# Optimization experiments

Measured on AMD Instinct MI355X. Metric: run time of the kernel, lower is better.

The kernel has to match this reference:

```python
import jax, jax.numpy as jnp
import numpy as np

DIM = 256
HEADS = 8
HD = DIM // HEADS        # head_dim = 32
WS = 8                   # window_size (Wh = Ww = 8)
NEXP = 8                 # num_experts
HID = 128                # attr_hidden_size (router hidden)
SCALE = HD ** -0.5


def _window_partition(x, ws):
    # (B, H, W, C) -> (B * H//ws * W//ws, ws, ws, C)
    B, H, W, C = x.shape
    x = x.reshape(B, H // ws, ws, W // ws, ws, C)
    return x.transpose(0, 1, 3, 2, 4, 5).reshape(-1, ws, ws, C)


def _window_reverse(w, ws, B, H, W):
    # inverse of _window_partition
    C = w.shape[-1]
    x = w.reshape(B, H // ws, W // ws, ws, ws, C)
    return x.transpose(0, 1, 3, 2, 4, 5).reshape(B, H, W, C)


def _rope2(x):
    # 2D rotary embedding over a window: x (B*, Wh, Ww, d).
    # First d/2 channels rotated by row position, last d/2 by column position.
    B, Wh, Ww, d = x.shape
    d2 = d // 2

    def angles(L, dd):
        inv = 1.0 / (10000.0 ** (jnp.arange(0, dd, 2, dtype=jnp.float32) / dd))
        return jnp.arange(L, dtype=jnp.float32)[:, None] * inv[None, :]  # (L, dd//2)

    def rotate(v, ang, bshape):
        # v: (B, Wh, Ww, dd) pairs interleaved; ang broadcast as bshape
        p = v.reshape(*v.shape[:-1], -1, 2)
        c = jnp.cos(ang).reshape(bshape)
        s = jnp.sin(ang).reshape(bshape)
        o0 = p[..., 0] * c - p[..., 1] * s
        o1 = p[..., 0] * s + p[..., 1] * c
        return jnp.stack([o0, o1], axis=-1).reshape(v.shape)

    ah = angles(Wh, d2)  # (Wh, d2//2)
    aw = angles(Ww, d2)  # (Ww, d2//2)
    xh = rotate(x[..., :d2], ah, (1, Wh, 1, d2 // 2))
    xw = rotate(x[..., d2:], aw, (1, 1, Ww, d2 // 2))
    return jnp.concatenate([xh, xw], axis=-1)


def _moe_linear(xf, routes, w, b):
    # Top-1 dispatch: per-expert dense GEMM, masked select (jit-safe, static shapes).
    # xf: (T, in), routes: (T,) int, w: (E, out, in), b: (E, out)
    out = jnp.zeros((xf.shape[0], w.shape[1]), xf.dtype)
    for i in range(w.shape[0]):
        y = xf @ w[i].T + b[i]
        out = jnp.where((routes == i)[:, None], y, out)
    return out


def setup_inputs() -> dict:
    key = jax.random.key(0)
    ks = jax.random.split(key, 8)
    sc = 0.02
    return {
        "x": jax.random.normal(ks[0], (8, 64, 64, DIM), jnp.float32),
        "router_w1": jax.random.normal(ks[1], (HID, DIM), jnp.float32) * sc,
        "router_b1": jnp.zeros((HID,), jnp.float32),
        "router_w2": jax.random.normal(ks[2], (NEXP, HID), jnp.float32) * sc,
        "router_b2": jnp.zeros((NEXP,), jnp.float32),
        "qkv_w": jax.random.normal(ks[3], (NEXP, 3 * DIM, DIM), jnp.float32) * sc,
        "qkv_b": jnp.zeros((NEXP, 3 * DIM), jnp.float32),
        "proj_w": jax.random.normal(ks[4], (NEXP, DIM, DIM), jnp.float32) * sc,
        "proj_b": jnp.zeros((NEXP, DIM), jnp.float32),
    }


def reference(x, router_w1, router_b1, router_w2, router_b2,
              qkv_w, qkv_b, proj_w, proj_b):
    Bs, H, W, C = x.shape
    xf = x.reshape(-1, C)  # (T, C), T = Bs*H*W

    # --- Top-1 router (eval mode: no noise, no token dropping) ---
    h = jax.nn.relu(xf @ router_w1.T + router_b1)
    router_logits = h @ router_w2.T + router_b2          # (T, E)
    router_probs = jax.nn.softmax(router_logits, axis=-1)
    route_prob_max = jnp.max(router_probs, axis=-1)       # (T,)
    routes = jnp.argmax(router_probs, axis=-1)            # (T,)

    # --- per-expert QKV projection (grouped dispatch) ---
    qkv = _moe_linear(xf, routes, qkv_w, qkv_b)           # (T, 3C)
    qkv = qkv.reshape(Bs, H, W, 3 * C)

    # --- window partition (shift=0, dilated=1 -> no roll, mask=None) ---
    qw = _window_partition(qkv, WS).reshape(-1, WS * WS, 3 * C)
    B_, N, _ = qw.shape
    qkv5 = qw.reshape(B_, N, 3, HEADS, HD).transpose(2, 0, 3, 1, 4)  # (3,B_,h,N,hd)
    q, k, v = qkv5[0], qkv5[1], qkv5[2]

    # --- RoPE on q, k over the 2D window ---
    q = _rope2(q.reshape(-1, WS, WS, HD)).reshape(B_, HEADS, N, HD)
    k = _rope2(k.reshape(-1, WS, WS, HD)).reshape(B_, HEADS, N, HD)

    # --- windowed attention (moe_mask is all zeros in eval: no drops) ---
    attn = jax.nn.softmax((q * SCALE) @ k.swapaxes(-2, -1), axis=-1)  # (B_,h,N,N)
    out = (attn @ v).swapaxes(1, 2).reshape(B_, N, C)

    # --- window reverse ---
    out = _window_reverse(out.reshape(-1, WS, WS, C), WS, Bs, H, W)

    # --- per-expert output projection + Switch-style prob scaling ---
    of = _moe_linear(out.reshape(-1, C), routes, proj_w, proj_b)
    of = of * route_prob_max[:, None]
    return of.reshape(Bs, H, W, C)
```

## Files before the change

### kernel.cpp

```cpp
#include <hip/hip_runtime.h>
#include <hip/hip_bf16.h>

typedef unsigned short u16;
typedef unsigned int u32;
typedef __attribute__((ext_vector_type(8))) short short8;
typedef __attribute__((ext_vector_type(4))) float f32x4;

#define T_TOK 32768
#define SCALE_ATT 0.17677669529663687f

__device__ __forceinline__ u16 f2bf(float f){
  u32 u = __float_as_uint(f);
  u32 r = u + 0x7fffu + ((u >> 16) & 1u);
  return (u16)(r >> 16);
}
__device__ __forceinline__ float bf2f(u16 h){
  return __uint_as_float(((u32)h) << 16);
}

__device__ __forceinline__ int xcd_swz(int flat, int nwg){
  return (flat & 7) * (nwg >> 3) + (flat >> 3);
}

__device__ __forceinline__ void gl16(const u16* g, u16* l){
  __builtin_amdgcn_global_load_lds(
      (const __attribute__((address_space(1))) u32*)g,
      (__attribute__((address_space(3))) u32*)l, 16, 0, 0);
}

__global__ __launch_bounds__(256) void k_prep_w1(
    const float* __restrict__ rw1, u16* __restrict__ w1h, u16* __restrict__ w1l)
{
  int i = blockIdx.x * 256 + threadIdx.x;
  float4 v = ((const float4*)rw1)[i];
  ushort4 h, l;
  h.x = f2bf(v.x); h.y = f2bf(v.y); h.z = f2bf(v.z); h.w = f2bf(v.w);
  l.x = f2bf(v.x - bf2f(h.x)); l.y = f2bf(v.y - bf2f(h.y));
  l.z = f2bf(v.z - bf2f(h.z)); l.w = f2bf(v.w - bf2f(h.w));
  ((ushort4*)w1h)[i] = h;
  ((ushort4*)w1l)[i] = l;
}

__global__ __launch_bounds__(256) void k_router(
    const float* __restrict__ x, const u16* __restrict__ w1h, const u16* __restrict__ w1l,
    const float* __restrict__ b1, const float* __restrict__ w2, const float* __restrict__ b2,
    int* __restrict__ routes, float* __restrict__ pmax, int* __restrict__ hist,
    u16* __restrict__ x_bf,
    const float* __restrict__ qkvw, u16* __restrict__ qw_bf,
    const float* __restrict__ projw, u16* __restrict__ pw_bf)
{
  __shared__ __align__(16) char smem[64*132*4];
  int tid = threadIdx.x;

  if (blockIdx.x >= 512){
    int b = blockIdx.x - 512;
    if (b < 1536){
      int i = b * 256 + tid;
      float4 v = ((const float4*)qkvw)[i];
      ushort4 o;
      o.x = f2bf(v.x); o.y = f2bf(v.y); o.z = f2bf(v.z); o.w = f2bf(v.w);
      ((ushort4*)qw_bf)[i] = o;
    } else {
      int i = (b - 1536) * 256 + tid;
      float4 v = ((const float4*)projw)[i];
      ushort4 o;
      o.x = f2bf(v.x); o.y = f2bf(v.y); o.z = f2bf(v.z); o.w = f2bf(v.w);
      ((ushort4*)pw_bf)[i] = o;
    }
    return;
  }

  u16* Ah = (u16*)smem;
  u16* Al = Ah + 2560;
  u16* Bh = Al + 2560;
  u16* Bl = Bh + 5120;
  float* Hs = (float*)smem;
  __shared__ int lhist[8];

  int t0 = blockIdx.x * 64;
  int wv = tid >> 6, lane = tid & 63, quad = lane >> 4, l16 = lane & 15;
  if (tid < 8) lhist[tid] = 0;

  int arow = tid >> 2, acg = tid & 3;
  int brow = tid >> 1, bhalf = tid & 1;

  f32x4 acc[4][2];
  #pragma unroll
  for (int i = 0; i < 4; ++i)
    #pragma unroll
    for (int j = 0; j < 2; ++j)
      #pragma unroll
      for (int rr = 0; rr < 4; ++rr) acc[i][j][rr] = 0.f;

  const float* gx_base = x + (size_t)(t0 + arow) * 256 + acg * 8;
  u16* gxb_base = x_bf + (size_t)(t0 + arow) * 256 + acg * 8;
  const u16* gwh_base = w1h + (size_t)brow * 256 + bhalf * 16;
  const u16* gwl_base = w1l + (size_t)brow * 256 + bhalf * 16;

  float4 v0 = *(const float4*)gx_base;
  float4 v1 = *(const float4*)(gx_base + 4);
  uint4 wh0 = *(const uint4*)(gwh_base);
  uint4 wh1 = *(const uint4*)(gwh_base + 8);
  uint4 wl0 = *(const uint4*)(gwl_base);
  uint4 wl1 = *(const uint4*)(gwl_base + 8);

  for (int kt = 0; kt < 8; ++kt){
    ushort4 h0, h1, l0, l1;
    h0.x = f2bf(v0.x); h0.y = f2bf(v0.y); h0.z = f2bf(v0.z); h0.w = f2bf(v0.w);
    h1.x = f2bf(v1.x); h1.y = f2bf(v1.y); h1.z = f2bf(v1.z); h1.w = f2bf(v1.w);
    l0.x = f2bf(v0.x - bf2f(h0.x)); l0.y = f2bf(v0.y - bf2f(h0.y));
    l0.z = f2bf(v0.z - bf2f(h0.z)); l0.w = f2bf(v0.w - bf2f(h0.w));
    l1.x = f2bf(v1.x - bf2f(h1.x)); l1.y = f2bf(v1.y - bf2f(h1.y));
    l1.z = f2bf(v1.z - bf2f(h1.z)); l1.w = f2bf(v1.w - bf2f(h1.w));
    *(ushort4*)(gxb_base + kt*32)     = h0;
    *(ushort4*)(gxb_base + kt*32 + 4) = h1;
    __syncthreads();
    *(ushort4*)&Ah[arow*40 + acg*8    ] = h0;
    *(ushort4*)&Ah[arow*40 + acg*8 + 4] = h1;
    *(ushort4*)&Al[arow*40 + acg*8    ] = l0;
    *(ushort4*)&Al[arow*40 + acg*8 + 4] = l1;
    *(uint4*)&Bh[brow*40 + bhalf*16    ] = wh0;
    *(uint4*)&Bh[brow*40 + bhalf*16 + 8] = wh1;
    *(uint4*)&Bl[brow*40 + bhalf*16    ] = wl0;
    *(uint4*)&Bl[brow*40 + bhalf*16 + 8] = wl1;
    __syncthreads();
    if (kt < 7){
      v0  = *(const float4*)(gx_base + (kt+1)*32);
      v1  = *(const float4*)(gx_base + (kt+1)*32 + 4);
      wh0 = *(const uint4*)(gwh_base + (kt+1)*32);
      wh1 = *(const uint4*)(gwh_base + (kt+1)*32 + 8);
      wl0 = *(const uint4*)(gwl_base + (kt+1)*32);
      wl1 = *(const uint4*)(gwl_base + (kt+1)*32 + 8);
    }
    short8 ah[4], al[4], bhf[2], blf[2];
    #pragma unroll
    for (int i = 0; i < 4; ++i){
      ah[i] = *(const short8*)&Ah[(i*16 + l16)*40 + quad*8];
      al[i] = *(const short8*)&Al[(i*16 + l16)*40 + quad*8];
    }
    #pragma unroll
    for (int j = 0; j < 2; ++j){
      bhf[j] = *(const short8*)&Bh[(wv*32 + j*16 + l16)*40 + quad*8];
      blf[j] = *(const short8*)&Bl[(wv*32 + j*16 + l16)*40 + quad*8];
    }
    #pragma unroll
    for (int i = 0; i < 4; ++i)
      #pragma unroll
      for (int j = 0; j < 2; ++j){
        acc[i][j] = __builtin_amdgcn_mfma_f32_16x16x32_bf16(ah[i], bhf[j], acc[i][j], 0, 0, 0);
        acc[i][j] = __builtin_amdgcn_mfma_f32_16x16x32_bf16(ah[i], blf[j], acc[i][j], 0, 0, 0);
        acc[i][j] = __builtin_amdgcn_mfma_f32_16x16x32_bf16(al[i], bhf[j], acc[i][j], 0, 0, 0);
      }
  }
  __syncthreads();

  #pragma unroll
  for (int i = 0; i < 4; ++i)
    #pragma unroll
    for (int j = 0; j < 2; ++j){
      int col = wv*32 + j*16 + l16;
      float bb = b1[col];
      #pragma unroll
      for (int rr = 0; rr < 4; ++rr){
        float h = acc[i][j][rr] + bb;
        Hs[(i*16 + quad*4 + rr)*132 + col] = h > 0.f ? h : 0.f;
      }
    }
  __syncthreads();

  #pragma unroll
  for (int pass = 0; pass < 2; ++pass){
    int mtok = (tid >> 3) + pass * 32;
    int e = tid & 7;
    const float4* w2r = (const float4*)(w2 + e * 128);
    float l = b2[e];
    #pragma unroll
    for (int k4 = 0; k4 < 32; ++k4){
      float4 w = w2r[k4];
      int k = k4 * 4;
      l = fmaf(Hs[mtok*132+k  ], w.x, l);
      l = fmaf(Hs[mtok*132+k+1], w.y, l);
      l = fmaf(Hs[mtok*132+k+2], w.z, l);
      l = fmaf(Hs[mtok*132+k+3], w.w, l);
    }
    float mv = l; int mi = e;
    #pragma unroll
    for (int off = 1; off < 8; off <<= 1){
      float ov = __shfl_xor(mv, off, 64);
      int   oi = __shfl_xor(mi, off, 64);
      if (ov > mv || (ov == mv && oi < mi)){ mv = ov; mi = oi; }
    }
    float sum = expf(l - mv);
    #pragma unroll
    for (int off = 1; off < 8; off <<= 1) sum += __shfl_xor(sum, off, 64);
    if (e == 0){
      int t = t0 + mtok;
      routes[t] = mi;
      pmax[t] = 1.0f / sum;
      atomicAdd(&lhist[mi], 1);
    }
  }
  __syncthreads();
  if (tid < 8) hist[blockIdx.x * 8 + tid] = lhist[tid];
}

__global__ __launch_bounds__(256) void k_scatter(
    const int* __restrict__ routes, const int* __restrict__ hist,
    int* __restrict__ sorted, int* __restrict__ rank, int* __restrict__ offs)
{
  __shared__ int s_tot[8], s_pre[8], so[9], lc[8];
  int tid = threadIdx.x, b = blockIdx.x;
  if (tid < 8){ s_tot[tid] = 0; s_pre[tid] = 0; lc[tid] = 0; }
  __syncthreads();
  int e8 = tid & 7, r0 = tid >> 3;
  int tot = 0, pre = 0;
  for (int rb = r0; rb < 512; rb += 32){
    int v = hist[rb * 8 + e8];
    tot += v;
    if (rb < b * 4) pre += v;
  }
  atomicAdd(&s_tot[e8], tot);
  atomicAdd(&s_pre[e8], pre);
  __syncthreads();
  if (tid == 0){
    int o = 0; so[0] = 0;
    #pragma unroll
    for (int e = 0; e < 8; ++e){ o += ((s_tot[e] + 127) >> 7) << 7; so[e+1] = o; }
  }
  __syncthreads();
  int t = b * 256 + tid;
  int e = routes[t];
  int rl = atomicAdd(&lc[e], 1);
  int pos = so[e] + s_pre[e] + rl;
  sorted[pos] = t;
  rank[t] = pos;
  if (b == 0){
    if (tid < 9) offs[tid] = so[tid];
    #pragma unroll
    for (int e2 = 0; e2 < 8; ++e2)
      for (int i = so[e2] + s_tot[e2] + tid; i < so[e2+1]; i += 256) sorted[i] = -1;
  }
}

template<int NOUT, bool PROJ, int NB, int NWG>
__global__ __launch_bounds__(256) void k_gemm(
    const u16* __restrict__ A, const u16* __restrict__ W,
    const float* __restrict__ bias, const int* __restrict__ sidx,
    const int* __restrict__ offs, const float* __restrict__ pmax,
    u16* __restrict__ outb, float* __restrict__ outf)
{
  __shared__ __align__(1024) u16 As[3][4096];
  __shared__ __align__(1024) u16 Bs[3][4096];
  int tid = threadIdx.x;
  int flat = blockIdx.y * NB + blockIdx.x;
  int logical = xcd_swz(flat, NWG);
  int m0 = (logical / NB) * 128;
  int n0 = (logical % NB) * 128;
  int total = offs[8];
  if (m0 >= total) return;
  int e = 0;
  #pragma unroll
  for (int i = 1; i < 8; ++i) if (m0 >= offs[i]) e = i;

  int wv = tid >> 6, lane = tid & 63, quad = lane >> 4, l16 = lane & 15;
  int wrow = (wv >> 1) * 64, wcol = (wv & 1) * 64;

  int srow = wv*16 + (lane >> 2);
  int cg = (lane & 3) ^ ((srow >> 1) & 3);
  const u16 *ag0, *ag1;
  if (PROJ){
    ag0 = A + (size_t)(m0 + srow) * 256 + cg * 8;
    ag1 = A + (size_t)(m0 + srow + 64) * 256 + cg * 8;
  } else {
    int tA0 = sidx[m0 + srow];      if (tA0 < 0) tA0 = 0;
    int tA1 = sidx[m0 + srow + 64]; if (tA1 < 0) tA1 = 0;
    ag0 = A + (size_t)tA0 * 256 + cg * 8;
    ag1 = A + (size_t)tA1 * 256 + cg * 8;
  }
  int pc = (srow >> 4) + (srow & 15) * 4;
  const u16* bg0 = W + ((size_t)e * NOUT + n0 + pc) * 256 + cg * 8;
  const u16* bg1 = W + ((size_t)e * NOUT + n0 + 64 + pc) * 256 + cg * 8;

  f32x4 acc[4][4];
  #pragma unroll
  for (int i = 0; i < 4; ++i)
    #pragma unroll
    for (int j = 0; j < 4; ++j)
      #pragma unroll
      for (int r = 0; r < 4; ++r) acc[i][j][r] = 0.f;

  int qsw8 = (quad ^ ((l16 >> 1) & 3)) * 8;

#define STAGE_KT(kt, buf) do { \
    u16* a_lo = (u16*)((char*)&As[(buf)][0] + wv*1024); \
    u16* b_lo = (u16*)((char*)&Bs[(buf)][0] + wv*1024); \
    gl16(ag0 + (kt)*32, a_lo); \
    gl16(ag1 + (kt)*32, (u16*)((char*)a_lo + 4096)); \
    gl16(bg0 + (kt)*32, b_lo); \
    gl16(bg1 + (kt)*32, (u16*)((char*)b_lo + 4096)); \
  } while(0)

  STAGE_KT(0, 0);
  STAGE_KT(1, 1);

  #pragma unroll
  for (int kt = 0; kt < 8; ++kt){
    const int cur = kt % 3;
    if (kt < 7) asm volatile("s_waitcnt vmcnt(4) lgkmcnt(0)" ::: "memory");
    else        asm volatile("s_waitcnt vmcnt(0) lgkmcnt(0)" ::: "memory");
    __builtin_amdgcn_sched_barrier(0);
    __builtin_amdgcn_s_barrier();
    __builtin_amdgcn_sched_barrier(0);
    if (kt < 6) STAGE_KT(kt+2, (kt+2)%3);
    short8 af[4], bfv[4];
    #pragma unroll
    for (int i = 0; i < 4; ++i)
      af[i] = *(const short8*)&As[cur][(wrow + i*16 + l16)*32 + qsw8];
    #pragma unroll
    for (int j = 0; j < 4; ++j)
      bfv[j] = *(const short8*)&Bs[cur][(wcol + j*16 + l16)*32 + qsw8];
    #pragma unroll
    for (int i = 0; i < 4; ++i)
      #pragma unroll
      for (int j = 0; j < 4; ++j)
        acc[i][j] = __builtin_amdgcn_mfma_f32_16x16x32_bf16(af[i], bfv[j], acc[i][j], 0, 0, 0);
  }
#undef STAGE_KT

  float4 bj4 = *(const float4*)&bias[e*NOUT + n0 + wcol + l16*4];
  if (PROJ){
    #pragma unroll
    for (int i = 0; i < 4; ++i){
      #pragma unroll
      for (int ri = 0; ri < 4; ++ri){
        int row = wrow + i*16 + quad*4 + ri;
        int t = sidx[m0 + row];
        if (t < 0) continue;
        float pm = pmax[t];
        float4 ov;
        ov.x = (acc[i][0][ri] + bj4.x) * pm;
        ov.y = (acc[i][1][ri] + bj4.y) * pm;
        ov.z = (acc[i][2][ri] + bj4.z) * pm;
        ov.w = (acc[i][3][ri] + bj4.w) * pm;
        *(float4*)&outf[(size_t)t * NOUT + n0 + wcol + l16*4] = ov;
      }
    }
  } else {
    int col0 = n0 + wcol + l16*4;
    bool isqk = (col0 < 512);
    float inv0 = 0.f, inv1 = 0.f;
    float qsc = (col0 < 256) ? SCALE_ATT : 1.0f;
    if (isqk){
      int p0 = (col0 & 15) >> 1;
      inv0 = __expf(-1.1512925465f * (float)p0);
      inv1 = inv0 * 0.31622776601683794f;
    }
    int sel  = col0 >> 8;
    int head = (col0 >> 5) & 7;
    int ch   = col0 & 31;
    size_t hb = ((size_t)(sel * 8 + head) * 512) * 2048 + ch;
    #pragma unroll
    for (int i = 0; i < 4; ++i){
      #pragma unroll
      for (int ri = 0; ri < 4; ++ri){
        int row = wrow + i*16 + quad*4 + ri;
        int t = sidx[m0 + row];
        if (t < 0) continue;
        float vx = acc[i][0][ri] + bj4.x;
        float vy = acc[i][1][ri] + bj4.y;
        float vz = acc[i][2][ri] + bj4.z;
        float vw = acc[i][3][ri] + bj4.w;
        if (isqk){
          float pos = (float)((col0 & 16) ? (t & 7) : ((t >> 6) & 7));
          float a0r = pos * inv0, a1r = pos * inv1;
          float s0, c0s, s1, c1s;
          __sincosf(a0r, &s0, &c0s);
          __sincosf(a1r, &s1, &c1s);
          float r0 = (vx*c0s - vy*s0) * qsc;
          float r1 = (vx*s0 + vy*c0s) * qsc;
          float r2 = (vz*c1s - vw*s1) * qsc;
          float r3 = (vz*s1 + vw*c1s) * qsc;
          vx = r0; vy = r1; vz = r2; vw = r3;
        }
        int win = (t >> 12) * 64 + ((t >> 9) & 7) * 8 + ((t >> 3) & 7);
        int n   = ((t >> 6) & 7) * 8 + (t & 7);
        uint2 ov;
        ov.x = (u32)f2bf(vx) | ((u32)f2bf(vy) << 16);
        ov.y = (u32)f2bf(vz) | ((u32)f2bf(vw) << 16);
        *(uint2*)&outb[hb + (size_t)win * 2048 + n * 32] = ov;
      }
    }
  }
}

__global__ __launch_bounds__(64, 3) void k_attn(const u16* __restrict__ qkv,
                                                const int* __restrict__ rank,
                                                u16* __restrict__ attn_s)
{
  __shared__ __align__(16) u16 Ps[64*72];
  __shared__ __align__(16) u16 Vt[32*72];

  int lane = threadIdx.x;
  int quad = lane >> 4, l16 = lane & 15;
  int wh = xcd_swz(blockIdx.x, 4096);
  int head = wh >> 9, win = wh & 511;
  int b = win >> 6, wy = (win >> 3) & 7, wx = win & 7;
  int tb = b*4096 + wy*512 + wx*8;

  const u16* qbase = qkv + (size_t)(head * 512 + win) * 2048;
  const u16* kbase = qbase + (size_t)8 * 512 * 2048;
  const u16* vbase = qbase + (size_t)16 * 512 * 2048;

  int rk[4][4];
  #pragma unroll
  for (int i = 0; i < 4; ++i)
    #pragma unroll
    for (int rr = 0; rr < 4; ++rr){
      int m = i*16 + quad*4 + rr;
      rk[i][rr] = rank[tb + (m >> 3) * 64 + (m & 7)];
    }

  short8 qf[4], kf[4];
  #pragma unroll
  for (int i = 0; i < 4; ++i){
    qf[i] = *(const short8*)(qbase + (i*16 + l16)*32 + quad*8);
    kf[i] = *(const short8*)(kbase + (i*16 + l16)*32 + quad*8);
  }
  uint4 va[4];
  #pragma unroll
  for (int h = 0; h < 4; ++h)
    va[h] = *(const uint4*)(vbase + h*512 + l16*32 + quad*8);

  f32x4 sa[4][4];
  #pragma unroll
  for (int i = 0; i < 4; ++i)
    #pragma unroll
    for (int j = 0; j < 4; ++j){
      #pragma unroll
      for (int rr = 0; rr < 4; ++rr) sa[i][j][rr] = 0.f;
      sa[i][j] = __builtin_amdgcn_mfma_f32_16x16x32_bf16(qf[i], kf[j], sa[i][j], 0, 0, 0);
    }

  f32x4 rs[4];
  #pragma unroll
  for (int i = 0; i < 4; ++i)
    #pragma unroll
    for (int rr = 0; rr < 4; ++rr){
      float e0 = __expf(sa[i][0][rr]);
      float e1 = __expf(sa[i][1][rr]);
      float e2 = __expf(sa[i][2][rr]);
      float e3 = __expf(sa[i][3][rr]);
      rs[i][rr] = (e0 + e1) + (e2 + e3);
      uint2 pk;
      pk.x = (u32)f2bf(e0) | ((u32)f2bf(e1) << 16);
      pk.y = (u32)f2bf(e2) | ((u32)f2bf(e3) << 16);
      *(uint2*)&Ps[(i*16 + quad*4 + rr)*72 + l16*4] = pk;
    }
  #pragma unroll
  for (int i = 0; i < 4; ++i)
    #pragma unroll
    for (int rr = 0; rr < 4; ++rr){
      #pragma unroll
      for (int off = 1; off < 16; off <<= 1)
        rs[i][rr] += __shfl_xor(rs[i][rr], off, 64);
    }

  u32* vu = (u32*)va;
  #pragma unroll
  for (int h = 0; h < 4; ++h){
    int pn = l16 * 4 + h;
    #pragma unroll
    for (int w = 0; w < 4; ++w){
      u32 vv = vu[h*4 + w];
      Vt[(quad*8 + 2*w    )*72 + pn] = (u16)(vv & 0xffff);
      Vt[(quad*8 + 2*w + 1)*72 + pn] = (u16)(vv >> 16);
    }
  }

  f32x4 oa[4][2];
  #pragma unroll
  for (int i = 0; i < 4; ++i)
    #pragma unroll
    for (int rr = 0; rr < 4; ++rr){ oa[i][0][rr] = 0.f; oa[i][1][rr] = 0.f; }
  #pragma unroll
  for (int ks = 0; ks < 2; ++ks){
    short8 vf0 = *(const short8*)&Vt[(     l16)*72 + ks*32 + quad*8];
    short8 vf1 = *(const short8*)&Vt[(16 + l16)*72 + ks*32 + quad*8];
    #pragma unroll
    for (int i = 0; i < 4; ++i){
      short8 pf = *(const short8*)&Ps[(i*16 + l16)*72 + ks*32 + quad*8];
      oa[i][0] = __builtin_amdgcn_mfma_f32_16x16x32_bf16(pf, vf0, oa[i][0], 0, 0, 0);
      oa[i][1] = __builtin_amdgcn_mfma_f32_16x16x32_bf16(pf, vf1, oa[i][1], 0, 0, 0);
    }
  }

  #pragma unroll
  for (int i = 0; i < 4; ++i)
    #pragma unroll
    for (int rr = 0; rr < 4; ++rr){
      float inv = __builtin_amdgcn_rcpf(rs[i][rr]);
      int pos = rk[i][rr];
      u16* op = attn_s + (size_t)pos * 256 + head * 32 + l16;
      op[0]  = f2bf(oa[i][0][rr] * inv);
      op[16] = f2bf(oa[i][1][rr] * inv);
    }
}

extern "C" void kernel_launch(void* const* d_in, const int* in_sizes, int n_in,
                              void* d_out, int out_size, void* d_ws, size_t ws_size,
                              hipStream_t stream){
  const float* x     = (const float*)d_in[0];
  const float* rw1   = (const float*)d_in[1];
  const float* rb1   = (const float*)d_in[2];
  const float* rw2   = (const float*)d_in[3];
  const float* rb2   = (const float*)d_in[4];
  const float* qkvw  = (const float*)d_in[5];
  const float* qkvb  = (const float*)d_in[6];
  const float* projw = (const float*)d_in[7];
  const float* projb = (const float*)d_in[8];
  float* out = (float*)d_out;

  char* ws = (char*)d_ws;
  u16*   x_bf    = (u16*)(ws);
  u16*   qkv_bf  = (u16*)(ws + 16777216);
  u16*   w1h     = (u16*)(ws + 67108864);
  u16*   w1l     = w1h + 32768;
  u16*   attn_s  = (u16*)(ws + 67108864);
  u16*   qw_bf   = (u16*)(ws + 84410368);
  u16*   pw_bf   = (u16*)(ws + 87556096);
  int*   routes  = (int*)(ws + 88604672);
  float* pmaxp   = (float*)(ws + 88735744);
  int*   sorted  = (int*)(ws + 88866816);
  int*   rank    = (int*)(ws + 89001984);
  int*   hist    = (int*)(ws + 89133056);
  int*   offs    = (int*)(ws + 89149440);

  k_prep_w1<<<32, 256, 0, stream>>>(rw1, w1h, w1l);
  k_router<<<2560, 256, 0, stream>>>(x, w1h, w1l, rb1, rw2, rb2, routes, pmaxp, hist,
                                     x_bf, qkvw, qw_bf, projw, pw_bf);
  k_scatter<<<128, 256, 0, stream>>>(routes, hist, sorted, rank, offs);
  k_gemm<768, false, 6, 1584><<<dim3(6, 264), 256, 0, stream>>>(
      x_bf, qw_bf, qkvb, sorted, offs, nullptr, qkv_bf, nullptr);
  k_attn<<<4096, 64, 0, stream>>>(qkv_bf, rank, attn_s);
  k_gemm<256, true, 2, 528><<<dim3(2, 264), 256, 0, stream>>>(
      attn_s, pw_bf, projb, sorted, offs, pmaxp, nullptr, out);
}
```

Before: 195.3 us.

## Widen grouped GEMM tile to 128x256 with interleaved column mapping

Doubles the N tile of the expert-grouped GEMM from 128 to 256 columns, so each wave now accumulates a 64x128 block and the A tile is reused across twice as many output columns. B rows are loaded with a permuted column mapping so each lane owns 8 contiguous output columns, which allows 16-byte bf16 stores and handles four RoPE frequency pairs per lane. The grid is halved, and launch bounds now request one block per CU. Register and LDS use per block grow, which lowers occupancy and may hurt latency hiding, and the smaller grid leaves fewer blocks to spread across CUs.

```diff
diff --git a/kernel.cpp b/kernel.cpp
--- a/kernel.cpp
+++ b/kernel.cpp
@@ -243,19 +243,19 @@
 }
 
 template<int NOUT, bool PROJ, int NB, int NWG>
-__global__ __launch_bounds__(256) void k_gemm(
+__global__ __launch_bounds__(256, 1) void k_gemm(
     const u16* __restrict__ A, const u16* __restrict__ W,
     const float* __restrict__ bias, const int* __restrict__ sidx,
     const int* __restrict__ offs, const float* __restrict__ pmax,
     u16* __restrict__ outb, float* __restrict__ outf)
 {
   __shared__ __align__(1024) u16 As[3][4096];
-  __shared__ __align__(1024) u16 Bs[3][4096];
+  __shared__ __align__(1024) u16 Bs[3][8192];
   int tid = threadIdx.x;
   int flat = blockIdx.y * NB + blockIdx.x;
   int logical = xcd_swz(flat, NWG);
   int m0 = (logical / NB) * 128;
-  int n0 = (logical % NB) * 128;
+  int n0 = (logical % NB) * 256;
   int total = offs[8];
   if (m0 >= total) return;
   int e = 0;
@@ -263,7 +263,7 @@
   for (int i = 1; i < 8; ++i) if (m0 >= offs[i]) e = i;
 
   int wv = tid >> 6, lane = tid & 63, quad = lane >> 4, l16 = lane & 15;
-  int wrow = (wv >> 1) * 64, wcol = (wv & 1) * 64;
+  int wrow = (wv >> 1) * 64, wcol = (wv & 1) * 128;
 
   int srow = wv*16 + (lane >> 2);
   int cg = (lane & 3) ^ ((srow >> 1) & 3);
@@ -277,57 +277,67 @@
     ag0 = A + (size_t)tA0 * 256 + cg * 8;
     ag1 = A + (size_t)tA1 * 256 + cg * 8;
   }
-  int pc = (srow >> 4) + (srow & 15) * 4;
-  const u16* bg0 = W + ((size_t)e * NOUT + n0 + pc) * 256 + cg * 8;
-  const u16* bg1 = W + ((size_t)e * NOUT + n0 + 64 + pc) * 256 + cg * 8;
-
-  f32x4 acc[4][4];
-  #pragma unroll
-  for (int i = 0; i < 4; ++i)
-    #pragma unroll
-    for (int j = 0; j < 4; ++j)
+  int pcb = (srow & 15) * 8 + (srow >> 4);
+  const u16* bg0 = W + ((size_t)e * NOUT + n0 +       pcb    ) * 256 + cg * 8;
+  const u16* bg1 = W + ((size_t)e * NOUT + n0 +       pcb + 4) * 256 + cg * 8;
+  const u16* bg2 = W + ((size_t)e * NOUT + n0 + 128 + pcb    ) * 256 + cg * 8;
+  const u16* bg3 = W + ((size_t)e * NOUT + n0 + 128 + pcb + 4) * 256 + cg * 8;
+
+  f32x4 acc[4][8];
+  #pragma unroll
+  for (int i = 0; i < 4; ++i)
+    #pragma unroll
+    for (int j = 0; j < 8; ++j)
       #pragma unroll
       for (int r = 0; r < 4; ++r) acc[i][j][r] = 0.f;
 
   int qsw8 = (quad ^ ((l16 >> 1) & 3)) * 8;
 
 #define STAGE_KT(kt, buf) do { \
-    u16* a_lo = (u16*)((char*)&As[(buf)][0] + wv*1024); \
-    u16* b_lo = (u16*)((char*)&Bs[(buf)][0] + wv*1024); \
+    u16* a_lo = &As[(buf)][0] + wv*512; \
+    u16* b_lo = &Bs[(buf)][0] + wv*512; \
     gl16(ag0 + (kt)*32, a_lo); \
-    gl16(ag1 + (kt)*32, (u16*)((char*)a_lo + 4096)); \
+    gl16(ag1 + (kt)*32, a_lo + 2048); \
     gl16(bg0 + (kt)*32, b_lo); \
-    gl16(bg1 + (kt)*32, (u16*)((char*)b_lo + 4096)); \
+    gl16(bg1 + (kt)*32, b_lo + 2048); \
+    gl16(bg2 + (kt)*32, b_lo + 4096); \
+    gl16(bg3 + (kt)*32, b_lo + 6144); \
   } while(0)
 
   STAGE_KT(0, 0);
+  __builtin_amdgcn_sched_barrier(0);
   STAGE_KT(1, 1);
+  __builtin_amdgcn_sched_barrier(0);
 
   #pragma unroll
   for (int kt = 0; kt < 8; ++kt){
     const int cur = kt % 3;
-    if (kt < 7) asm volatile("s_waitcnt vmcnt(4) lgkmcnt(0)" ::: "memory");
+    if (kt < 7) asm volatile("s_waitcnt vmcnt(6) lgkmcnt(0)" ::: "memory");
     else        asm volatile("s_waitcnt vmcnt(0) lgkmcnt(0)" ::: "memory");
     __builtin_amdgcn_sched_barrier(0);
     __builtin_amdgcn_s_barrier();
     __builtin_amdgcn_sched_barrier(0);
-    if (kt < 6) STAGE_KT(kt+2, (kt+2)%3);
-    short8 af[4], bfv[4];
+    if (kt < 6){
+      STAGE_KT(kt+2, (kt+2)%3);
+      __builtin_amdgcn_sched_barrier(0);
+    }
+    short8 af[4];
     #pragma unroll
     for (int i = 0; i < 4; ++i)
       af[i] = *(const short8*)&As[cur][(wrow + i*16 + l16)*32 + qsw8];
     #pragma unroll
-    for (int j = 0; j < 4; ++j)
-      bfv[j] = *(const short8*)&Bs[cur][(wcol + j*16 + l16)*32 + qsw8];
-    #pragma unroll
-    for (int i = 0; i < 4; ++i)
-      #pragma unroll
-      for (int j = 0; j < 4; ++j)
-        acc[i][j] = __builtin_amdgcn_mfma_f32_16x16x32_bf16(af[i], bfv[j], acc[i][j], 0, 0, 0);
+    for (int j = 0; j < 8; ++j){
+      short8 bf = *(const short8*)&Bs[cur][(wcol + j*16 + l16)*32 + qsw8];
+      #pragma unroll
+      for (int i = 0; i < 4; ++i)
+        acc[i][j] = __builtin_amdgcn_mfma_f32_16x16x32_bf16(af[i], bf, acc[i][j], 0, 0, 0);
+    }
   }
 #undef STAGE_KT
 
-  float4 bj4 = *(const float4*)&bias[e*NOUT + n0 + wcol + l16*4];
+  int col0 = n0 + wcol + l16*8;
+  float4 bj0 = *(const float4*)&bias[e*NOUT + col0];
+  float4 bj1 = *(const float4*)&bias[e*NOUT + col0 + 4];
   if (PROJ){
     #pragma unroll
     for (int i = 0; i < 4; ++i){
@@ -337,27 +347,32 @@
         int t = sidx[m0 + row];
         if (t < 0) continue;
         float pm = pmax[t];
-        float4 ov;
-        ov.x = (acc[i][0][ri] + bj4.x) * pm;
-        ov.y = (acc[i][1][ri] + bj4.y) * pm;
-        ov.z = (acc[i][2][ri] + bj4.z) * pm;
-        ov.w = (acc[i][3][ri] + bj4.w) * pm;
-        *(float4*)&outf[(size_t)t * NOUT + n0 + wcol + l16*4] = ov;
+        float4 o0, o1;
+        o0.x = (acc[i][0][ri] + bj0.x) * pm;
+        o0.y = (acc[i][1][ri] + bj0.y) * pm;
+        o0.z = (acc[i][2][ri] + bj0.z) * pm;
+        o0.w = (acc[i][3][ri] + bj0.w) * pm;
+        o1.x = (acc[i][4][ri] + bj1.x) * pm;
+        o1.y = (acc[i][5][ri] + bj1.y) * pm;
+        o1.z = (acc[i][6][ri] + bj1.z) * pm;
+        o1.w = (acc[i][7][ri] + bj1.w) * pm;
+        *(float4*)&outf[(size_t)t * NOUT + col0    ] = o0;
+        *(float4*)&outf[(size_t)t * NOUT + col0 + 4] = o1;
       }
     }
   } else {
-    int col0 = n0 + wcol + l16*4;
     bool isqk = (col0 < 512);
-    float inv0 = 0.f, inv1 = 0.f;
-    float qsc = (col0 < 256) ? SCALE_ATT : 1.0f;
-    if (isqk){
-      int p0 = (col0 & 15) >> 1;
-      inv0 = __expf(-1.1512925465f * (float)p0);
-      inv1 = inv0 * 0.31622776601683794f;
-    }
     int sel  = col0 >> 8;
     int head = (col0 >> 5) & 7;
     int ch   = col0 & 31;
+    float qsc = (col0 < 256) ? SCALE_ATT : 1.0f;
+    float inv0 = 0.f, inv1 = 0.f, inv2 = 0.f, inv3 = 0.f;
+    if (isqk){
+      int p0 = (ch & 15) >> 1;
+      const float rstep = 0.31622776601683794f;
+      inv0 = __expf(-1.1512925465f * (float)p0);
+      inv1 = inv0 * rstep; inv2 = inv1 * rstep; inv3 = inv2 * rstep;
+    }
     size_t hb = ((size_t)(sel * 8 + head) * 512) * 2048 + ch;
     #pragma unroll
     for (int i = 0; i < 4; ++i){
@@ -366,28 +381,35 @@
         int row = wrow + i*16 + quad*4 + ri;
         int t = sidx[m0 + row];
         if (t < 0) continue;
-        float vx = acc[i][0][ri] + bj4.x;
-        float vy = acc[i][1][ri] + bj4.y;
-        float vz = acc[i][2][ri] + bj4.z;
-        float vw = acc[i][3][ri] + bj4.w;
+        float v0 = acc[i][0][ri] + bj0.x;
+        float v1 = acc[i][1][ri] + bj0.y;
+        float v2 = acc[i][2][ri] + bj0.z;
+        float v3 = acc[i][3][ri] + bj0.w;
+        float v4 = acc[i][4][ri] + bj1.x;
+        float v5 = acc[i][5][ri] + bj1.y;
+        float v6 = acc[i][6][ri] + bj1.z;
+        float v7 = acc[i][7][ri] + bj1.w;
         if (isqk){
-          float pos = (float)((col0 & 16) ? (t & 7) : ((t >> 6) & 7));
-          float a0r = pos * inv0, a1r = pos * inv1;
-          float s0, c0s, s1, c1s;
-          __sincosf(a0r, &s0, &c0s);
-          __sincosf(a1r, &s1, &c1s);
-          float r0 = (vx*c0s - vy*s0) * qsc;
-          float r1 = (vx*s0 + vy*c0s) * qsc;
-          float r2 = (vz*c1s - vw*s1) * qsc;
-          float r3 = (vz*s1 + vw*c1s) * qsc;
-          vx = r0; vy = r1; vz = r2; vw = r3;
+          float pos = (float)((ch & 16) ? (t & 7) : ((t >> 6) & 7));
+          float s0,c0,s1,c1,s2,c2,s3,c3;
+          __sincosf(pos * inv0, &s0, &c0);
+          __sincosf(pos * inv1, &s1, &c1);
+          __sincosf(pos * inv2, &s2, &c2);
+          __sincosf(pos * inv3, &s3, &c3);
+          float r0 = (v0*c0 - v1*s0) * qsc, r1 = (v0*s0 + v1*c0) * qsc;
+          float r2 = (v2*c1 - v3*s1) * qsc, r3 = (v2*s1 + v3*c1) * qsc;
+          float r4 = (v4*c2 - v5*s2) * qsc, r5 = (v4*s2 + v5*c2) * qsc;
+          float r6 = (v6*c3 - v7*s3) * qsc, r7 = (v6*s3 + v7*c3) * qsc;
+          v0=r0; v1=r1; v2=r2; v3=r3; v4=r4; v5=r5; v6=r6; v7=r7;
         }
         int win = (t >> 12) * 64 + ((t >> 9) & 7) * 8 + ((t >> 3) & 7);
         int n   = ((t >> 6) & 7) * 8 + (t & 7);
-        uint2 ov;
-        ov.x = (u32)f2bf(vx) | ((u32)f2bf(vy) << 16);
-        ov.y = (u32)f2bf(vz) | ((u32)f2bf(vw) << 16);
-        *(uint2*)&outb[hb + (size_t)win * 2048 + n * 32] = ov;
+        uint4 ov;
+        ov.x = (u32)f2bf(v0) | ((u32)f2bf(v1) << 16);
+        ov.y = (u32)f2bf(v2) | ((u32)f2bf(v3) << 16);
+        ov.z = (u32)f2bf(v4) | ((u32)f2bf(v5) << 16);
+        ov.w = (u32)f2bf(v6) | ((u32)f2bf(v7) << 16);
+        *(uint4*)&outb[hb + (size_t)win * 2048 + n * 32] = ov;
       }
     }
   }
@@ -539,9 +561,9 @@
   k_router<<<2560, 256, 0, stream>>>(x, w1h, w1l, rb1, rw2, rb2, routes, pmaxp, hist,
                                      x_bf, qkvw, qw_bf, projw, pw_bf);
   k_scatter<<<128, 256, 0, stream>>>(routes, hist, sorted, rank, offs);
-  k_gemm<768, false, 6, 1584><<<dim3(6, 264), 256, 0, stream>>>(
+  k_gemm<768, false, 3, 792><<<dim3(3, 264), 256, 0, stream>>>(
       x_bf, qw_bf, qkvb, sorted, offs, nullptr, qkv_bf, nullptr);
   k_attn<<<4096, 64, 0, stream>>>(qkv_bf, rank, attn_s);
-  k_gemm<256, true, 2, 528><<<dim3(2, 264), 256, 0, stream>>>(
+  k_gemm<256, true, 1, 264><<<dim3(1, 264), 256, 0, stream>>>(
       attn_s, pw_bf, projb, sorted, offs, pmaxp, nullptr, out);
 }
```

Measured after the change: 198.2 us. No clear change (+1.5%).

## Fuse windowed attention with per-expert output projection in one kernel

Applied to the files above, without the earlier changes.

Merges the attention kernel and the expert-sorted output-projection GEMM into a single kernel: each 512-thread block handles one window with all 8 heads, stages the attention output in LDS with an XOR swizzle, then loops over the experts present in the window and runs MFMA projection masked by a ballot of routes. This drops the rank array, the attn_s round trip through global memory and one kernel launch. The proj weights are pre-permuted into an MFMA fragment layout during conversion. The cost is that the projection is computed once for every distinct expert in each window, and the large LDS footprint limits occupancy to one block per CU.

```diff
diff --git a/kernel.cpp b/kernel.cpp
--- a/kernel.cpp
+++ b/kernel.cpp
@@ -65,7 +65,14 @@
       float4 v = ((const float4*)projw)[i];
       ushort4 o;
       o.x = f2bf(v.x); o.y = f2bf(v.y); o.z = f2bf(v.z); o.w = f2bf(v.w);
-      ((ushort4*)pw_bf)[i] = o;
+      int f = i * 4;
+      int e  = f >> 16;
+      int n  = (f >> 8) & 255;
+      int k  = f & 255;
+      int kt = k >> 5, quad = (k >> 3) & 3, el = k & 7;
+      int nf = n >> 4, l16 = n & 15;
+      size_t dst = ((((size_t)(e*8 + kt)*16 + nf)*16 + l16)*4 + quad)*8 + el;
+      *(ushort4*)&pw_bf[dst] = o;
     }
     return;
   }
@@ -206,7 +213,7 @@
 
 __global__ __launch_bounds__(256) void k_scatter(
     const int* __restrict__ routes, const int* __restrict__ hist,
-    int* __restrict__ sorted, int* __restrict__ rank, int* __restrict__ offs)
+    int* __restrict__ sorted, int* __restrict__ offs)
 {
   __shared__ int s_tot[8], s_pre[8], so[9], lc[8];
   int tid = threadIdx.x, b = blockIdx.x;
@@ -233,7 +240,6 @@
   int rl = atomicAdd(&lc[e], 1);
   int pos = so[e] + s_pre[e] + rl;
   sorted[pos] = t;
-  rank[t] = pos;
   if (b == 0){
     if (tid < 9) offs[tid] = so[tid];
     #pragma unroll
@@ -242,12 +248,12 @@
   }
 }
 
-template<int NOUT, bool PROJ, int NB, int NWG>
+template<int NOUT, int NB, int NWG>
 __global__ __launch_bounds__(256) void k_gemm(
     const u16* __restrict__ A, const u16* __restrict__ W,
     const float* __restrict__ bias, const int* __restrict__ sidx,
-    const int* __restrict__ offs, const float* __restrict__ pmax,
-    u16* __restrict__ outb, float* __restrict__ outf)
+    const int* __restrict__ offs,
+    u16* __restrict__ outb)
 {
   __shared__ __align__(1024) u16 As[3][4096];
   __shared__ __align__(1024) u16 Bs[3][4096];
@@ -267,16 +273,10 @@
 
   int srow = wv*16 + (lane >> 2);
   int cg = (lane & 3) ^ ((srow >> 1) & 3);
-  const u16 *ag0, *ag1;
-  if (PROJ){
-    ag0 = A + (size_t)(m0 + srow) * 256 + cg * 8;
-    ag1 = A + (size_t)(m0 + srow + 64) * 256 + cg * 8;
-  } else {
-    int tA0 = sidx[m0 + srow];      if (tA0 < 0) tA0 = 0;
-    int tA1 = sidx[m0 + srow + 64]; if (tA1 < 0) tA1 = 0;
-    ag0 = A + (size_t)tA0 * 256 + cg * 8;
-    ag1 = A + (size_t)tA1 * 256 + cg * 8;
-  }
+  int tA0 = sidx[m0 + srow];      if (tA0 < 0) tA0 = 0;
+  int tA1 = sidx[m0 + srow + 64]; if (tA1 < 0) tA1 = 0;
+  const u16* ag0 = A + (size_t)tA0 * 256 + cg * 8;
+  const u16* ag1 = A + (size_t)tA1 * 256 + cg * 8;
   int pc = (srow >> 4) + (srow & 15) * 4;
   const u16* bg0 = W + ((size_t)e * NOUT + n0 + pc) * 256 + cg * 8;
   const u16* bg1 = W + ((size_t)e * NOUT + n0 + 64 + pc) * 256 + cg * 8;
@@ -292,16 +292,18 @@
   int qsw8 = (quad ^ ((l16 >> 1) & 3)) * 8;
 
 #define STAGE_KT(kt, buf) do { \
-    u16* a_lo = (u16*)((char*)&As[(buf)][0] + wv*1024); \
-    u16* b_lo = (u16*)((char*)&Bs[(buf)][0] + wv*1024); \
+    u16* a_lo = &As[(buf)][0] + wv*512; \
+    u16* b_lo = &Bs[(buf)][0] + wv*512; \
     gl16(ag0 + (kt)*32, a_lo); \
-    gl16(ag1 + (kt)*32, (u16*)((char*)a_lo + 4096)); \
+    gl16(ag1 + (kt)*32, a_lo + 2048); \
     gl16(bg0 + (kt)*32, b_lo); \
-    gl16(bg1 + (kt)*32, (u16*)((char*)b_lo + 4096)); \
+    gl16(bg1 + (kt)*32, b_lo + 2048); \
   } while(0)
 
   STAGE_KT(0, 0);
+  __builtin_amdgcn_sched_barrier(0);
   STAGE_KT(1, 1);
+  __builtin_amdgcn_sched_barrier(0);
 
   #pragma unroll
   for (int kt = 0; kt < 8; ++kt){
@@ -311,7 +313,10 @@
     __builtin_amdgcn_sched_barrier(0);
     __builtin_amdgcn_s_barrier();
     __builtin_amdgcn_sched_barrier(0);
-    if (kt < 6) STAGE_KT(kt+2, (kt+2)%3);
+    if (kt < 6){
+      STAGE_KT(kt+2, (kt+2)%3);
+      __builtin_amdgcn_sched_barrier(0);
+    }
     short8 af[4], bfv[4];
     #pragma unroll
     for (int i = 0; i < 4; ++i)
@@ -328,97 +333,81 @@
 #undef STAGE_KT
 
   float4 bj4 = *(const float4*)&bias[e*NOUT + n0 + wcol + l16*4];
-  if (PROJ){
-    #pragma unroll
-    for (int i = 0; i < 4; ++i){
-      #pragma unroll
-      for (int ri = 0; ri < 4; ++ri){
-        int row = wrow + i*16 + quad*4 + ri;
-        int t = sidx[m0 + row];
-        if (t < 0) continue;
-        float pm = pmax[t];
-        float4 ov;
-        ov.x = (acc[i][0][ri] + bj4.x) * pm;
-        ov.y = (acc[i][1][ri] + bj4.y) * pm;
-        ov.z = (acc[i][2][ri] + bj4.z) * pm;
-        ov.w = (acc[i][3][ri] + bj4.w) * pm;
-        *(float4*)&outf[(size_t)t * NOUT + n0 + wcol + l16*4] = ov;
+  int col0 = n0 + wcol + l16*4;
+  bool isqk = (col0 < 512);
+  float inv0 = 0.f, inv1 = 0.f;
+  float qsc = (col0 < 256) ? SCALE_ATT : 1.0f;
+  if (isqk){
+    int p0 = (col0 & 15) >> 1;
+    inv0 = __expf(-1.1512925465f * (float)p0);
+    inv1 = inv0 * 0.31622776601683794f;
+  }
+  int sel  = col0 >> 8;
+  int head = (col0 >> 5) & 7;
+  int ch   = col0 & 31;
+  size_t hb = ((size_t)(sel * 8 + head) * 512) * 2048 + ch;
+  #pragma unroll
+  for (int i = 0; i < 4; ++i){
+    #pragma unroll
+    for (int ri = 0; ri < 4; ++ri){
+      int row = wrow + i*16 + quad*4 + ri;
+      int t = sidx[m0 + row];
+      if (t < 0) continue;
+      float vx = acc[i][0][ri] + bj4.x;
+      float vy = acc[i][1][ri] + bj4.y;
+      float vz = acc[i][2][ri] + bj4.z;
+      float vw = acc[i][3][ri] + bj4.w;
+      if (isqk){
+        float pos = (float)((col0 & 16) ? (t & 7) : ((t >> 6) & 7));
+        float a0r = pos * inv0, a1r = pos * inv1;
+        float s0, c0s, s1, c1s;
+        __sincosf(a0r, &s0, &c0s);
+        __sincosf(a1r, &s1, &c1s);
+        float r0 = (vx*c0s - vy*s0) * qsc;
+        float r1 = (vx*s0 + vy*c0s) * qsc;
+        float r2 = (vz*c1s - vw*s1) * qsc;
+        float r3 = (vz*s1 + vw*c1s) * qsc;
+        vx = r0; vy = r1; vz = r2; vw = r3;
       }
-    }
-  } else {
-    int col0 = n0 + wcol + l16*4;
-    bool isqk = (col0 < 512);
-    float inv0 = 0.f, inv1 = 0.f;
-    float qsc = (col0 < 256) ? SCALE_ATT : 1.0f;
-    if (isqk){
-      int p0 = (col0 & 15) >> 1;
-      inv0 = __expf(-1.1512925465f * (float)p0);
-      inv1 = inv0 * 0.31622776601683794f;
-    }
-    int sel  = col0 >> 8;
-    int head = (col0 >> 5) & 7;
-    int ch   = col0 & 31;
-    size_t hb = ((size_t)(sel * 8 + head) * 512) * 2048 + ch;
-    #pragma unroll
-    for (int i = 0; i < 4; ++i){
-      #pragma unroll
-      for (int ri = 0; ri < 4; ++ri){
-        int row = wrow + i*16 + quad*4 + ri;
-        int t = sidx[m0 + row];
-        if (t < 0) continue;
-        float vx = acc[i][0][ri] + bj4.x;
-        float vy = acc[i][1][ri] + bj4.y;
-        float vz = acc[i][2][ri] + bj4.z;
-        float vw = acc[i][3][ri] + bj4.w;
-        if (isqk){
-          float pos = (float)((col0 & 16) ? (t & 7) : ((t >> 6) & 7));
-          float a0r = pos * inv0, a1r = pos * inv1;
-          float s0, c0s, s1, c1s;
-          __sincosf(a0r, &s0, &c0s);
-          __sincosf(a1r, &s1, &c1s);
-          float r0 = (vx*c0s - vy*s0) * qsc;
-          float r1 = (vx*s0 + vy*c0s) * qsc;
-          float r2 = (vz*c1s - vw*s1) * qsc;
-          float r3 = (vz*s1 + vw*c1s) * qsc;
-          vx = r0; vy = r1; vz = r2; vw = r3;
-        }
-        int win = (t >> 12) * 64 + ((t >> 9) & 7) * 8 + ((t >> 3) & 7);
-        int n   = ((t >> 6) & 7) * 8 + (t & 7);
-        uint2 ov;
-        ov.x = (u32)f2bf(vx) | ((u32)f2bf(vy) << 16);
-        ov.y = (u32)f2bf(vz) | ((u32)f2bf(vw) << 16);
-        *(uint2*)&outb[hb + (size_t)win * 2048 + n * 32] = ov;
-      }
-    }
-  }
-}
-
-__global__ __launch_bounds__(64, 3) void k_attn(const u16* __restrict__ qkv,
-                                                const int* __restrict__ rank,
-                                                u16* __restrict__ attn_s)
+      int win = (t >> 12) * 64 + ((t >> 9) & 7) * 8 + ((t >> 3) & 7);
+      int n   = ((t >> 6) & 7) * 8 + (t & 7);
+      uint2 ov;
+      ov.x = (u32)f2bf(vx) | ((u32)f2bf(vy) << 16);
+      ov.y = (u32)f2bf(vz) | ((u32)f2bf(vw) << 16);
+      *(uint2*)&outb[hb + (size_t)win * 2048 + n * 32] = ov;
+    }
+  }
+}
+
+__global__ __launch_bounds__(512, 1) void k_attn_proj(
+    const u16* __restrict__ qkv, const int* __restrict__ routes,
+    const float* __restrict__ pmax, const u16* __restrict__ pw,
+    const float* __restrict__ projb, float* __restrict__ out)
 {
-  __shared__ __align__(16) u16 Ps[64*72];
-  __shared__ __align__(16) u16 Vt[32*72];
-
-  int lane = threadIdx.x;
+  __shared__ __align__(16) u16 lds[55296];
+  __shared__ int er_s[64];
+  __shared__ float pm_s[64];
+
+  int tid = threadIdx.x;
+  int w = tid >> 6, lane = tid & 63;
   int quad = lane >> 4, l16 = lane & 15;
-  int wh = xcd_swz(blockIdx.x, 4096);
-  int head = wh >> 9, win = wh & 511;
+  u16* Ps = lds + w * 6912;
+  u16* Vt = Ps + 4608;
+  u16* O_s = lds;
+
+  int win = xcd_swz(blockIdx.x, 512);
   int b = win >> 6, wy = (win >> 3) & 7, wx = win & 7;
   int tb = b*4096 + wy*512 + wx*8;
 
-  const u16* qbase = qkv + (size_t)(head * 512 + win) * 2048;
+  if (tid < 64){
+    int t = tb + (tid >> 3) * 64 + (tid & 7);
+    er_s[tid] = routes[t];
+    pm_s[tid] = pmax[t];
+  }
+
+  const u16* qbase = qkv + (size_t)(w * 512 + win) * 2048;
   const u16* kbase = qbase + (size_t)8 * 512 * 2048;
   const u16* vbase = qbase + (size_t)16 * 512 * 2048;
-
-  int rk[4][4];
-  #pragma unroll
-  for (int i = 0; i < 4; ++i)
-    #pragma unroll
-    for (int rr = 0; rr < 4; ++rr){
-      int m = i*16 + quad*4 + rr;
-      rk[i][rr] = rank[tb + (m >> 3) * 64 + (m & 7)];
-    }
 
   short8 qf[4], kf[4];
   #pragma unroll
@@ -470,10 +459,10 @@
   for (int h = 0; h < 4; ++h){
     int pn = l16 * 4 + h;
     #pragma unroll
-    for (int w = 0; w < 4; ++w){
-      u32 vv = vu[h*4 + w];
-      Vt[(quad*8 + 2*w    )*72 + pn] = (u16)(vv & 0xffff);
-      Vt[(quad*8 + 2*w + 1)*72 + pn] = (u16)(vv >> 16);
+    for (int ww = 0; ww < 4; ++ww){
+      u32 vv = vu[h*4 + ww];
+      Vt[(quad*8 + 2*ww    )*72 + pn] = (u16)(vv & 0xffff);
+      Vt[(quad*8 + 2*ww + 1)*72 + pn] = (u16)(vv >> 16);
     }
   }
 
@@ -494,16 +483,59 @@
     }
   }
 
+  __syncthreads();
+
   #pragma unroll
   for (int i = 0; i < 4; ++i)
     #pragma unroll
     for (int rr = 0; rr < 4; ++rr){
       float inv = __builtin_amdgcn_rcpf(rs[i][rr]);
-      int pos = rk[i][rr];
-      u16* op = attn_s + (size_t)pos * 256 + head * 32 + l16;
-      op[0]  = f2bf(oa[i][0][rr] * inv);
-      op[16] = f2bf(oa[i][1][rr] * inv);
-    }
+      int m = i*16 + quad*4 + rr;
+      int key = (m & 7) << 3;
+      int c0 = w*32 + l16;
+      O_s[m*256 + (c0 ^ key)]        = f2bf(oa[i][0][rr] * inv);
+      O_s[m*256 + ((c0+16) ^ key)]   = f2bf(oa[i][1][rr] * inv);
+    }
+  __syncthreads();
+
+  int e_l = er_s[lane];
+  #pragma unroll 1
+  for (int eu = 0; eu < 8; ++eu){
+    unsigned long long hit = __ballot(e_l == eu);
+    if (hit == 0ull) continue;
+    float b0 = projb[eu*256 + w*32 + l16];
+    float b1 = projb[eu*256 + w*32 + 16 + l16];
+    f32x4 acc[4][2];
+    #pragma unroll
+    for (int i = 0; i < 4; ++i)
+      #pragma unroll
+      for (int r = 0; r < 4; ++r){ acc[i][0][r] = 0.f; acc[i][1][r] = 0.f; }
+    #pragma unroll
+    for (int kt = 0; kt < 8; ++kt){
+      const u16* bb = pw + ((((size_t)(eu*8 + kt)*16 + w*2)*16 + l16)*4 + quad)*8;
+      short8 bf0 = *(const short8*)bb;
+      short8 bf1 = *(const short8*)(bb + 512);
+      int ck = (kt*32 + quad*8);
+      #pragma unroll
+      for (int i = 0; i < 4; ++i){
+        int row = i*16 + l16;
+        short8 af = *(const short8*)&O_s[row*256 + (ck ^ ((row & 7) << 3))];
+        acc[i][0] = __builtin_amdgcn_mfma_f32_16x16x32_bf16(af, bf0, acc[i][0], 0, 0, 0);
+        acc[i][1] = __builtin_amdgcn_mfma_f32_16x16x32_bf16(af, bf1, acc[i][1], 0, 0, 0);
+      }
+    }
+    #pragma unroll
+    for (int i = 0; i < 4; ++i)
+      #pragma unroll
+      for (int ri = 0; ri < 4; ++ri){
+        int row = i*16 + quad*4 + ri;
+        if (!((hit >> row) & 1ull)) continue;
+        int t = tb + (row >> 3) * 64 + (row & 7);
+        float pm = pm_s[row];
+        out[(size_t)t * 256 + w*32 + l16]      = (acc[i][0][ri] + b0) * pm;
+        out[(size_t)t * 256 + w*32 + 16 + l16] = (acc[i][1][ri] + b1) * pm;
+      }
+  }
 }
 
 extern "C" void kernel_launch(void* const* d_in, const int* in_sizes, int n_in,
@@ -525,23 +557,19 @@
   u16*   qkv_bf  = (u16*)(ws + 16777216);
   u16*   w1h     = (u16*)(ws + 67108864);
   u16*   w1l     = w1h + 32768;
-  u16*   attn_s  = (u16*)(ws + 67108864);
   u16*   qw_bf   = (u16*)(ws + 84410368);
   u16*   pw_bf   = (u16*)(ws + 87556096);
   int*   routes  = (int*)(ws + 88604672);
   float* pmaxp   = (float*)(ws + 88735744);
   int*   sorted  = (int*)(ws + 88866816);
-  int*   rank    = (int*)(ws + 89001984);
   int*   hist    = (int*)(ws + 89133056);
   int*   offs    = (int*)(ws + 89149440);
 
   k_prep_w1<<<32, 256, 0, stream>>>(rw1, w1h, w1l);
   k_router<<<2560, 256, 0, stream>>>(x, w1h, w1l, rb1, rw2, rb2, routes, pmaxp, hist,
                                      x_bf, qkvw, qw_bf, projw, pw_bf);
-  k_scatter<<<128, 256, 0, stream>>>(routes, hist, sorted, rank, offs);
-  k_gemm<768, false, 6, 1584><<<dim3(6, 264), 256, 0, stream>>>(
-      x_bf, qw_bf, qkvb, sorted, offs, nullptr, qkv_bf, nullptr);
-  k_attn<<<4096, 64, 0, stream>>>(qkv_bf, rank, attn_s);
-  k_gemm<256, true, 2, 528><<<dim3(2, 264), 256, 0, stream>>>(
-      attn_s, pw_bf, projb, sorted, offs, pmaxp, nullptr, out);
-}
+  k_scatter<<<128, 256, 0, stream>>>(routes, hist, sorted, offs);
+  k_gemm<768, 6, 1584><<<dim3(6, 264), 256, 0, stream>>>(
+      x_bf, qw_bf, qkvb, sorted, offs, qkv_bf);
+  k_attn_proj<<<512, 512, 0, stream>>>(qkv_bf, routes, pmaxp, pw_bf, projb, out);
+}
```

Result: slower. 230.8 us (+18.2%).
